# Optimization experiments

Measured on AMD Instinct MI355X. Metric: run time of the kernel, lower is better.

Reference implementation:

```python
import jax, jax.numpy as jnp
import numpy as np

B, S, D, H, E = 4, 2048, 512, 1024, 8


def setup_inputs() -> dict:
    key = jax.random.key(0)
    ks = jax.random.split(key, 4)
    x = jax.random.normal(ks[0], (B, S, D), jnp.float32)
    Wr = jax.random.normal(ks[1], (E, D), jnp.float32) * 0.02   # router weight [E, D]
    br = jnp.zeros((E,), jnp.float32)
    W1 = jax.random.normal(ks[2], (E, D, H), jnp.float32) * 0.02  # fc1 per expert
    b1 = jnp.zeros((E, H), jnp.float32)
    W2 = jax.random.normal(ks[3], (E, H, D), jnp.float32) * 0.02  # fc2 per expert
    b2 = jnp.zeros((E, D), jnp.float32)
    return {"x": x, "Wr": Wr, "br": br, "W1": W1, "b1": b1, "W2": W2, "b2": b2}


def reference(x, Wr, br, W1, b1, W2, b2):
    # world_size == 1: every all_to_all is the identity; the pipeline reduces to
    # y[t] = sum_{k in top2} gate_k(t) * Expert_{idx_k(t)}(x[t])
    b, s, d = x.shape
    n = b * s
    e = Wr.shape[0]
    xf = x.reshape(n, d)                                   # (N, D)
    logits = xf @ Wr.T + br                                # (N, E)
    probs = jax.nn.softmax(logits, axis=-1)
    top2_prob, top2_idx = jax.lax.top_k(probs, 2)          # (N, 2) each, same tie-break as torch.topk
    # combine weights: comb[t, e] = sum_k gate_tk * [idx_tk == e]
    comb = jnp.zeros((n, e), x.dtype).at[jnp.arange(n)[:, None], top2_idx].add(top2_prob)
    # dense grouped-expert FFN (exact erf-GELU, matching torch F.gelu default)
    h = jax.nn.gelu(jnp.einsum('nd,edh->enh', xf, W1) + b1[:, None, :], approximate=False)
    o = jnp.einsum('enh,ehd->end', h, W2) + b2[:, None, :]  # (E, N, D)
    y = jnp.einsum('ne,end->nd', comb, o)                   # gate-weighted combine
    return y.reshape(b, s, d)
```

## Files before the change

kernel.cpp:

```cpp
#include <hip/hip_runtime.h>
#include <hip/hip_bf16.h>
#include <math.h>

#define N_TOK 8192
#define DIM   512
#define HID   1024
#define NEXP  8
#define CSTRIDE 32
#define NBLK  32
#define TCAP  80

typedef __attribute__((ext_vector_type(8))) __bf16 bf16x8;
typedef __attribute__((ext_vector_type(4))) float  f32x4;

static __device__ __forceinline__ unsigned short f2bf(float f) {
    unsigned int u = __builtin_bit_cast(unsigned int, f);
    unsigned int r = u + 0x7fffu + ((u >> 16) & 1u);
    return (unsigned short)(r >> 16);
}
static __device__ __forceinline__ float bf2f(unsigned short s) {
    unsigned int u = ((unsigned int)s) << 16;
    return __builtin_bit_cast(float, u);
}

__global__ __launch_bounds__(256) void prep_router_kernel(
    const float* __restrict__ x, const float* __restrict__ Wr,
    const float* __restrict__ br,
    const float* __restrict__ W1, const float* __restrict__ W2,
    unsigned short* __restrict__ xb,
    unsigned short* __restrict__ W1p, unsigned short* __restrict__ W2p,
    int* __restrict__ counts, int* __restrict__ tlist, float* __restrict__ glist)
{
    __shared__ unsigned short lt[32][128];
    __shared__ int lcnt[8];
    __shared__ int lbase[8];
    int bid = blockIdx.x;
    int tin = threadIdx.x;
    if (bid < 256) {
        int slot = tin >> 3, es = tin & 7;
        int t0 = bid * 32;
        int t = t0 + slot;
        if (tin < 8) lcnt[tin] = 0;
        const float4* xr = (const float4*)(x + (size_t)t * DIM + es * 64);
        float4 xv[16];
        #pragma unroll
        for (int i = 0; i < 16; i++) xv[i] = xr[i];
        float part[8];
        #pragma unroll
        for (int ed = 0; ed < 8; ed++) {
            const float4* wrp = (const float4*)(Wr + (size_t)ed * DIM + es * 64);
            float a = 0.f;
            #pragma unroll
            for (int i = 0; i < 16; i++) {
                float4 b = wrp[i];
                a += xv[i].x*b.x + xv[i].y*b.y + xv[i].z*b.z + xv[i].w*b.w;
            }
            part[ed] = a;
        }
        #pragma unroll
        for (int m = 1; m < 8; m <<= 1) {
            #pragma unroll
            for (int ed = 0; ed < 8; ed++)
                part[ed] += __shfl_xor(part[ed], m, 64);
        }
        int i1 = 0, i2 = 0, l1 = 0, l2 = 0;
        float p1 = 0.f, p2 = 0.f;
        __syncthreads();
        if (es == 0) {
            float l0[8];
            #pragma unroll
            for (int i = 0; i < 8; i++) l0[i] = part[i] + br[i];
            float m1v = l0[0];
            #pragma unroll
            for (int i = 1; i < 8; i++) if (l0[i] > m1v) { m1v = l0[i]; i1 = i; }
            float sum = 0.f;
            #pragma unroll
            for (int i = 0; i < 8; i++) sum += expf(l0[i] - m1v);
            float m2v = -1e30f;
            #pragma unroll
            for (int i = 0; i < 8; i++) if (i != i1 && l0[i] > m2v) { m2v = l0[i]; i2 = i; }
            float inv = 1.f / sum;
            p1 = inv;
            p2 = expf(m2v - m1v) * inv;
            l1 = atomicAdd(&lcnt[i1], 1);
            l2 = atomicAdd(&lcnt[i2], 1);
        }
        __syncthreads();
        if (tin < 8) lbase[tin] = atomicAdd(&counts[tin * CSTRIDE], lcnt[tin]);
        __syncthreads();
        if (es == 0) {
            int pos1 = lbase[i1] + l1;
            tlist[i1 * N_TOK + pos1] = t * 2;     glist[i1 * N_TOK + pos1] = p1;
            int pos2 = lbase[i2] + l2;
            tlist[i2 * N_TOK + pos2] = t * 2 + 1; glist[i2 * N_TOK + pos2] = p2;
        }
        #pragma unroll
        for (int i = 0; i < 8; i++) {
            int flat = i * 256 + tin;
            int row = flat >> 6, c8 = flat & 63;
            const float4* src = (const float4*)(x + (size_t)(t0 + row) * DIM + c8 * 8);
            float4 a = src[0], b = src[1];
            unsigned short u[8];
            u[0]=f2bf(a.x); u[1]=f2bf(a.y); u[2]=f2bf(a.z); u[3]=f2bf(a.w);
            u[4]=f2bf(b.x); u[5]=f2bf(b.y); u[6]=f2bf(b.z); u[7]=f2bf(b.w);
            *reinterpret_cast<uint4*>(xb + (size_t)(t0 + row) * DIM + c8 * 8) =
                *reinterpret_cast<const uint4*>(u);
        }
        return;
    }
    int e, kb, seg, OUTD;
    const float* W;
    bool isW1 = bid < 1280;
    if (isW1) {
        int b = bid - 256;
        e = b & 7; kb = (b >> 3) & 15; seg = b >> 7;
        OUTD = HID;
        W = W1 + (size_t)e * DIM * HID + (size_t)(kb * 32) * HID + seg * 128;
    } else {
        int b = bid - 1280;
        e = b & 7; kb = (b >> 3) & 31; seg = b >> 8;
        OUTD = DIM;
        W = W2 + (size_t)e * HID * DIM + (size_t)(kb * 32) * DIM + seg * 128;
    }
    #pragma unroll
    for (int i = 0; i < 4; i++) {
        int fl = i * 256 + tin;
        int r = fl >> 5, c4 = fl & 31;
        float4 v = *reinterpret_cast<const float4*>(W + (size_t)r * OUTD + c4 * 4);
        lt[r][c4*4+0] = f2bf(v.x); lt[r][c4*4+1] = f2bf(v.y);
        lt[r][c4*4+2] = f2bf(v.z); lt[r][c4*4+3] = f2bf(v.w);
    }
    __syncthreads();
    unsigned short* dstp = isW1 ? W1p : W2p;
    #pragma unroll
    for (int i = 0; i < 2; i++) {
        int s = i * 256 + tin;
        int nbl = s >> 6, l = s & 63;
        unsigned short u[8];
        #pragma unroll
        for (int j = 0; j < 8; j++) u[j] = lt[(l >> 4) * 8 + j][nbl * 16 + (l & 15)];
        size_t o;
        if (isW1) o = (((size_t)(e * 64 + seg * 8 + nbl) * 16 + kb) * 64 + l) * 8;
        else      o = (((size_t)(e * 32 + seg * 8 + nbl) * 32 + kb) * 64 + l) * 8;
        *reinterpret_cast<uint4*>(dstp + o) = *reinterpret_cast<const uint4*>(u);
    }
}

__global__ __launch_bounds__(512, 2) void ffn_kernel(
    const unsigned short* __restrict__ xb,
    const unsigned short* __restrict__ W1p,
    const unsigned short* __restrict__ W2p,
    const float* __restrict__ b1, const float* __restrict__ b2,
    const int* __restrict__ counts, const int* __restrict__ tlist,
    const float* __restrict__ glist, unsigned short* __restrict__ opair)
{
    const int e = blockIdx.x;
    const int cnt = counts[e * CSTRIDE];
    const int ty = blockIdx.y;
    const int m0 = (cnt * ty) >> 5;
    const int m1 = (cnt * (ty + 1)) >> 5;
    const int nvalid = m1 - m0;
    if (nvalid <= 0) return;

    __shared__ __align__(16) unsigned short xs[TCAP * 512];
    __shared__ __align__(16) unsigned short hs[2][TCAP * 256];

    const int tid = threadIdx.x;
    const int w = tid >> 6, lane = tid & 63;
    const int lg_ = lane >> 4, lm = lane & 15;
    const int tbase = e * N_TOK + m0;

    #pragma unroll
    for (int i = 0; i < 10; i++) {
        int row = w * 10 + i;
        uint4 v;
        if (row < nvalid) {
            int token = tlist[tbase + row] >> 1;
            v = *(reinterpret_cast<const uint4*>(xb + (size_t)token * DIM) + lane);
        } else {
            v.x = v.y = v.z = v.w = 0u;
        }
        int bo = row * 1024 + ((lane * 16) ^ ((row & 7) << 4));
        *reinterpret_cast<uint4*>(reinterpret_cast<char*>(xs) + bo) = v;
    }
    __syncthreads();

    const char* xsb = reinterpret_cast<const char*>(xs);

    f32x4 acc2[4][5];
    #pragma unroll
    for (int a = 0; a < 4; a++)
        #pragma unroll
        for (int b = 0; b < 5; b++) acc2[a][b] = (f32x4)0.f;

    const uint4* w1base = reinterpret_cast<const uint4*>(W1p)
        + ((size_t)(e * 64 + w * 2) * 16) * 64 + lane;
    bf16x8 aw1_pf[2];
    #pragma unroll
    for (int i = 0; i < 2; i++)
        aw1_pf[i] = __builtin_bit_cast(bf16x8, w1base[(size_t)(i * 16) * 64]);

    for (int c = 0; c < 4; c++) {
        char* hsb = reinterpret_cast<char*>(hs[c & 1]);
        f32x4 acc1[2][5];
        #pragma unroll
        for (int a = 0; a < 2; a++)
            #pragma unroll
            for (int b = 0; b < 5; b++) acc1[a][b] = (f32x4)0.f;
        #pragma unroll
        for (int kb = 0; kb < 16; kb++) {
            bf16x8 aw[2];
            #pragma unroll
            for (int i = 0; i < 2; i++)
                aw[i] = (kb == 0) ? aw1_pf[i]
                      : __builtin_bit_cast(bf16x8, w1base[(size_t)(i * 16 + kb) * 64]);
            #pragma unroll
            for (int tt = 0; tt < 5; tt++) {
                int row = tt * 16 + lm;
                int bo = row * 1024 + ((kb * 64 + lg_ * 16) ^ ((row & 7) << 4));
                bf16x8 bx = __builtin_bit_cast(bf16x8,
                    *reinterpret_cast<const uint4*>(xsb + bo));
                #pragma unroll
                for (int i = 0; i < 2; i++)
                    acc1[i][tt] = __builtin_amdgcn_mfma_f32_16x16x32_bf16(aw[i], bx, acc1[i][tt], 0, 0, 0);
            }
        }
        #pragma unroll
        for (int i = 0; i < 2; i++) {
            int hloc0 = (w * 2 + i) * 16 + lg_ * 4;
            f32x4 b1v = *reinterpret_cast<const f32x4*>(b1 + (size_t)e * HID + c * 256 + hloc0);
            #pragma unroll
            for (int tt = 0; tt < 5; tt++) {
                int trow = tt * 16 + lm;
                float g[4];
                #pragma unroll
                for (int r = 0; r < 4; r++) {
                    float v = acc1[i][tt][r] + b1v[r];
                    g[r] = 0.5f * v * (1.f + erff(v * 0.7071067811865475f));
                }
                unsigned int p0 = (unsigned int)f2bf(g[0]) | ((unsigned int)f2bf(g[1]) << 16);
                unsigned int p1 = (unsigned int)f2bf(g[2]) | ((unsigned int)f2bf(g[3]) << 16);
                unsigned long long pk = (unsigned long long)p0 | ((unsigned long long)p1 << 32);
                int bo = trow * 512 + ((hloc0 * 2) ^ ((trow & 7) << 4));
                *reinterpret_cast<unsigned long long*>(hsb + bo) = pk;
            }
        }
        const uint4* w2base = reinterpret_cast<const uint4*>(W2p)
            + ((size_t)(e * 32 + w * 4) * 32 + c * 8) * 64 + lane;
        bf16x8 aw2_pf[4];
        #pragma unroll
        for (int j = 0; j < 4; j++)
            aw2_pf[j] = __builtin_bit_cast(bf16x8, w2base[(size_t)(j * 32) * 64]);
        __syncthreads();
        if (c < 3) {
            w1base = reinterpret_cast<const uint4*>(W1p)
                + ((size_t)(e * 64 + (c + 1) * 16 + w * 2) * 16) * 64 + lane;
            #pragma unroll
            for (int i = 0; i < 2; i++)
                aw1_pf[i] = __builtin_bit_cast(bf16x8, w1base[(size_t)(i * 16) * 64]);
        }
        #pragma unroll
        for (int kb = 0; kb < 8; kb++) {
            bf16x8 aw2[4];
            #pragma unroll
            for (int j = 0; j < 4; j++)
                aw2[j] = (kb == 0) ? aw2_pf[j]
                       : __builtin_bit_cast(bf16x8, w2base[(size_t)(j * 32 + kb) * 64]);
            #pragma unroll
            for (int tt = 0; tt < 5; tt++) {
                int row = tt * 16 + lm;
                int bo = row * 512 + ((kb * 64 + lg_ * 16) ^ ((row & 7) << 4));
                bf16x8 bh = __builtin_bit_cast(bf16x8,
                    *reinterpret_cast<const uint4*>(reinterpret_cast<const char*>(hs[c & 1]) + bo));
                #pragma unroll
                for (int j = 0; j < 4; j++)
                    acc2[j][tt] = __builtin_amdgcn_mfma_f32_16x16x32_bf16(aw2[j], bh, acc2[j][tt], 0, 0, 0);
            }
        }
    }

    int   ent[5];
    float gt[5];
    #pragma unroll
    for (int tt = 0; tt < 5; tt++) {
        int trow = tt * 16 + lm;
        int src = (trow < nvalid) ? trow : 0;
        ent[tt] = tlist[tbase + src];
        gt[tt]  = glist[tbase + src];
    }
    #pragma unroll
    for (int j = 0; j < 4; j++) {
        int dbase = (w * 4 + j) * 16 + lg_ * 4;
        f32x4 b2v = *reinterpret_cast<const f32x4*>(b2 + (size_t)e * DIM + dbase);
        #pragma unroll
        for (int tt = 0; tt < 5; tt++) {
            int trow = tt * 16 + lm;
            if (trow < nvalid) {
                float o0 = gt[tt] * (acc2[j][tt][0] + b2v[0]);
                float o1 = gt[tt] * (acc2[j][tt][1] + b2v[1]);
                float o2 = gt[tt] * (acc2[j][tt][2] + b2v[2]);
                float o3 = gt[tt] * (acc2[j][tt][3] + b2v[3]);
                uint2 pk;
                pk.x = (unsigned int)f2bf(o0) | ((unsigned int)f2bf(o1) << 16);
                pk.y = (unsigned int)f2bf(o2) | ((unsigned int)f2bf(o3) << 16);
                *reinterpret_cast<uint2*>(opair + (size_t)ent[tt] * DIM + dbase) = pk;
            }
        }
    }
}

__global__ __launch_bounds__(256) void combine_kernel(
    const unsigned short* __restrict__ opair, float* __restrict__ y)
{
    int n = blockIdx.x * 256 + threadIdx.x;
    int t = n >> 6, c8 = n & 63;
    uint4 a = *reinterpret_cast<const uint4*>(opair + (size_t)(t * 2) * DIM + c8 * 8);
    uint4 b = *reinterpret_cast<const uint4*>(opair + (size_t)(t * 2 + 1) * DIM + c8 * 8);
    float4 r0, r1;
    r0.x = bf2f((unsigned short)(a.x      )) + bf2f((unsigned short)(b.x      ));
    r0.y = bf2f((unsigned short)(a.x >> 16)) + bf2f((unsigned short)(b.x >> 16));
    r0.z = bf2f((unsigned short)(a.y      )) + bf2f((unsigned short)(b.y      ));
    r0.w = bf2f((unsigned short)(a.y >> 16)) + bf2f((unsigned short)(b.y >> 16));
    r1.x = bf2f((unsigned short)(a.z      )) + bf2f((unsigned short)(b.z      ));
    r1.y = bf2f((unsigned short)(a.z >> 16)) + bf2f((unsigned short)(b.z >> 16));
    r1.z = bf2f((unsigned short)(a.w      )) + bf2f((unsigned short)(b.w      ));
    r1.w = bf2f((unsigned short)(a.w >> 16)) + bf2f((unsigned short)(b.w >> 16));
    float4* dst = reinterpret_cast<float4*>(y + (size_t)t * DIM + c8 * 8);
    dst[0] = r0; dst[1] = r1;
}

extern "C" void kernel_launch(void* const* d_in, const int* in_sizes, int n_in,
                              void* d_out, int out_size, void* d_ws, size_t ws_size,
                              hipStream_t stream)
{
    const float* x  = (const float*)d_in[0];
    const float* Wr = (const float*)d_in[1];
    const float* br = (const float*)d_in[2];
    const float* W1 = (const float*)d_in[3];
    const float* b1 = (const float*)d_in[4];
    const float* W2 = (const float*)d_in[5];
    const float* b2 = (const float*)d_in[6];
    float* y = (float*)d_out;

    char* ws = (char*)d_ws;
    int*   counts = (int*)ws;
    int*   tlist  = (int*)(ws + 1024);
    float* glist  = (float*)(ws + 1024 + 262144);
    unsigned short* xb  = (unsigned short*)(ws + 1024 + 524288);
    unsigned short* W1p = xb  + (size_t)N_TOK * DIM;
    unsigned short* W2p = W1p + (size_t)NEXP * DIM * HID;
    unsigned short* opair = W2p + (size_t)NEXP * HID * DIM;

    hipMemsetAsync(counts, 0, NEXP * CSTRIDE * sizeof(int), stream);
    prep_router_kernel<<<2304, 256, 0, stream>>>(x, Wr, br, W1, W2, xb,
                                                 W1p, W2p, counts, tlist, glist);
    ffn_kernel<<<dim3(8, NBLK), 512, 0, stream>>>(xb, W1p, W2p, b1, b2,
                                                  counts, tlist, glist, opair);
    combine_kernel<<<2048, 256, 0, stream>>>(opair, y);
}
```

Measured before the change: 104.9 us.

## Fuse top-2 combine into FFN epilogue via fp32 atomic adds into zeroed output

The separate combine kernel and the bf16 per-pair intermediate buffer are removed. The router/prep kernel now zeroes y, and the FFN epilogue atomically adds gate-weighted fp32 expert outputs straight into y. This saves a kernel launch and a round trip through the pair buffer, and it drops the bf16 rounding of partial outputs. In exchange, every output element takes two scalar global float atomics, which may be slower than packed stores, and the order of the two additions is not fixed.

```diff
diff --git a/kernel.cpp b/kernel.cpp
--- a/kernel.cpp
+++ b/kernel.cpp
@@ -18,10 +18,6 @@
     unsigned int r = u + 0x7fffu + ((u >> 16) & 1u);
     return (unsigned short)(r >> 16);
 }
-static __device__ __forceinline__ float bf2f(unsigned short s) {
-    unsigned int u = ((unsigned int)s) << 16;
-    return __builtin_bit_cast(float, u);
-}
 
 __global__ __launch_bounds__(256) void prep_router_kernel(
     const float* __restrict__ x, const float* __restrict__ Wr,
@@ -29,7 +25,8 @@
     const float* __restrict__ W1, const float* __restrict__ W2,
     unsigned short* __restrict__ xb,
     unsigned short* __restrict__ W1p, unsigned short* __restrict__ W2p,
-    int* __restrict__ counts, int* __restrict__ tlist, float* __restrict__ glist)
+    int* __restrict__ counts, int* __restrict__ tlist, float* __restrict__ glist,
+    float* __restrict__ y)
 {
     __shared__ unsigned short lt[32][128];
     __shared__ int lcnt[8];
@@ -94,6 +91,7 @@
             int pos2 = lbase[i2] + l2;
             tlist[i2 * N_TOK + pos2] = t * 2 + 1; glist[i2 * N_TOK + pos2] = p2;
         }
+        float4 z4; z4.x = z4.y = z4.z = z4.w = 0.f;
         #pragma unroll
         for (int i = 0; i < 8; i++) {
             int flat = i * 256 + tin;
@@ -105,6 +103,8 @@
             u[4]=f2bf(b.x); u[5]=f2bf(b.y); u[6]=f2bf(b.z); u[7]=f2bf(b.w);
             *reinterpret_cast<uint4*>(xb + (size_t)(t0 + row) * DIM + c8 * 8) =
                 *reinterpret_cast<const uint4*>(u);
+            float4* yd = reinterpret_cast<float4*>(y + (size_t)(t0 + row) * DIM + c8 * 8);
+            yd[0] = z4; yd[1] = z4;
         }
         return;
     }
@@ -152,7 +152,7 @@
     const unsigned short* __restrict__ W2p,
     const float* __restrict__ b1, const float* __restrict__ b2,
     const int* __restrict__ counts, const int* __restrict__ tlist,
-    const float* __restrict__ glist, unsigned short* __restrict__ opair)
+    const float* __restrict__ glist, float* __restrict__ y)
 {
     const int e = blockIdx.x;
     const int cnt = counts[e * CSTRIDE];
@@ -279,13 +279,13 @@
         }
     }
 
-    int   ent[5];
+    int   tok[5];
     float gt[5];
     #pragma unroll
     for (int tt = 0; tt < 5; tt++) {
         int trow = tt * 16 + lm;
         int src = (trow < nvalid) ? trow : 0;
-        ent[tt] = tlist[tbase + src];
+        tok[tt] = tlist[tbase + src] >> 1;
         gt[tt]  = glist[tbase + src];
     }
     #pragma unroll
@@ -296,37 +296,13 @@
         for (int tt = 0; tt < 5; tt++) {
             int trow = tt * 16 + lm;
             if (trow < nvalid) {
-                float o0 = gt[tt] * (acc2[j][tt][0] + b2v[0]);
-                float o1 = gt[tt] * (acc2[j][tt][1] + b2v[1]);
-                float o2 = gt[tt] * (acc2[j][tt][2] + b2v[2]);
-                float o3 = gt[tt] * (acc2[j][tt][3] + b2v[3]);
-                uint2 pk;
-                pk.x = (unsigned int)f2bf(o0) | ((unsigned int)f2bf(o1) << 16);
-                pk.y = (unsigned int)f2bf(o2) | ((unsigned int)f2bf(o3) << 16);
-                *reinterpret_cast<uint2*>(opair + (size_t)ent[tt] * DIM + dbase) = pk;
-            }
-        }
-    }
-}
-
-__global__ __launch_bounds__(256) void combine_kernel(
-    const unsigned short* __restrict__ opair, float* __restrict__ y)
-{
-    int n = blockIdx.x * 256 + threadIdx.x;
-    int t = n >> 6, c8 = n & 63;
-    uint4 a = *reinterpret_cast<const uint4*>(opair + (size_t)(t * 2) * DIM + c8 * 8);
-    uint4 b = *reinterpret_cast<const uint4*>(opair + (size_t)(t * 2 + 1) * DIM + c8 * 8);
-    float4 r0, r1;
-    r0.x = bf2f((unsigned short)(a.x      )) + bf2f((unsigned short)(b.x      ));
-    r0.y = bf2f((unsigned short)(a.x >> 16)) + bf2f((unsigned short)(b.x >> 16));
-    r0.z = bf2f((unsigned short)(a.y      )) + bf2f((unsigned short)(b.y      ));
-    r0.w = bf2f((unsigned short)(a.y >> 16)) + bf2f((unsigned short)(b.y >> 16));
-    r1.x = bf2f((unsigned short)(a.z      )) + bf2f((unsigned short)(b.z      ));
-    r1.y = bf2f((unsigned short)(a.z >> 16)) + bf2f((unsigned short)(b.z >> 16));
-    r1.z = bf2f((unsigned short)(a.w      )) + bf2f((unsigned short)(b.w      ));
-    r1.w = bf2f((unsigned short)(a.w >> 16)) + bf2f((unsigned short)(b.w >> 16));
-    float4* dst = reinterpret_cast<float4*>(y + (size_t)t * DIM + c8 * 8);
-    dst[0] = r0; dst[1] = r1;
+                float* yp = y + (size_t)tok[tt] * DIM + dbase;
+                #pragma unroll
+                for (int r = 0; r < 4; r++)
+                    atomicAdd(yp + r, gt[tt] * (acc2[j][tt][r] + b2v[r]));
+            }
+        }
+    }
 }
 
 extern "C" void kernel_launch(void* const* d_in, const int* in_sizes, int n_in,
@@ -349,12 +325,10 @@
     unsigned short* xb  = (unsigned short*)(ws + 1024 + 524288);
     unsigned short* W1p = xb  + (size_t)N_TOK * DIM;
     unsigned short* W2p = W1p + (size_t)NEXP * DIM * HID;
-    unsigned short* opair = W2p + (size_t)NEXP * HID * DIM;
 
     hipMemsetAsync(counts, 0, NEXP * CSTRIDE * sizeof(int), stream);
     prep_router_kernel<<<2304, 256, 0, stream>>>(x, Wr, br, W1, W2, xb,
-                                                 W1p, W2p, counts, tlist, glist);
+                                                 W1p, W2p, counts, tlist, glist, y);
     ffn_kernel<<<dim3(8, NBLK), 512, 0, stream>>>(xb, W1p, W2p, b1, b2,
-                                                  counts, tlist, glist, opair);
-    combine_kernel<<<2048, 256, 0, stream>>>(opair, y);
+                                                  counts, tlist, glist, y);
 }
```

After: 189.8 us. 1.81x slower.
